# Performance work log

Measured on AMD Instinct MI355X. Metric: run time of the kernel, lower is better.

The kernel has to match this reference:

```python
import jax, jax.numpy as jnp
import numpy as np

VERY_NEGATIVE_NUMBER = -1e29

B, TC, TQ, D = 32, 2048, 256, 256


def setup_inputs() -> dict:
    key = jax.random.key(0)
    k1, k2, k3, k4 = jax.random.split(key, 4)
    context_repr = jax.random.normal(k1, (B, TC, D), dtype=jnp.float32)
    question_repr = jax.random.normal(k2, (B, TQ, D), dtype=jnp.float32)
    # lengths in [1, maxlen] so no row is fully masked
    context_len = jax.random.randint(k3, (B,), 1, TC + 1, dtype=jnp.int32)
    question_len = jax.random.randint(k4, (B,), 1, TQ + 1, dtype=jnp.int32)
    return {
        "context_repr": context_repr,
        "question_repr": question_repr,
        "context_len": context_len,
        "question_len": question_len,
    }


def reference(context_repr, question_repr, context_len, question_len):
    dtype = context_repr.dtype
    Tc = context_repr.shape[1]
    Tq = question_repr.shape[1]
    # similarity: dot product over feature dim -> [B, Tc, Tq]
    sim_mat = jnp.einsum("bcd,bqd->bcq", context_repr, question_repr)
    # sequence masks
    cmask = (jnp.arange(Tc)[None, :] < context_len[:, None]).astype(dtype)  # [B,Tc]
    qmask = (jnp.arange(Tq)[None, :] < question_len[:, None]).astype(dtype)  # [B,Tq]
    mask = cmask[:, :, None] * qmask[:, None, :]  # [B,Tc,Tq]
    sim_mat = sim_mat + (1.0 - mask) * VERY_NEGATIVE_NUMBER
    # context-to-query attention
    c2q_prob = jax.nn.softmax(sim_mat, axis=-1)  # [B,Tc,Tq]
    context2query_attention = jnp.einsum("bcq,bqd->bcd", c2q_prob, question_repr)
    # query-to-context attention: row-wise max then softmax over context positions
    q2c_prob = jax.nn.softmax(jnp.max(sim_mat, axis=-1), axis=-1)  # [B,Tc]
    q2c = jnp.einsum("bc,bcd->bd", q2c_prob, context_repr)  # [B,D]
    query2context_attention = jnp.broadcast_to(
        q2c[:, None, :], context2query_attention.shape
    )
    return (context2query_attention, query2context_attention)
```

## Files before the change

kernel.cpp:

```cpp
#include <hip/hip_runtime.h>
#include <hip/hip_fp16.h>

#define DEVI __device__ __forceinline__

typedef float f32x4 __attribute__((ext_vector_type(4)));
typedef float float4v __attribute__((ext_vector_type(4)));
typedef _Float16 f16x8 __attribute__((ext_vector_type(8)));
typedef unsigned short us8 __attribute__((ext_vector_type(8)));

constexpr int NB = 32, TC = 2048, TQ = 256, DD = 256;
constexpr int CR = 64;
constexpr float VNEG = -1e29f;

DEVI unsigned short f2h(float f) {
  _Float16 h = (_Float16)f;
  return __builtin_bit_cast(unsigned short, h);
}
DEVI float h2f(unsigned short u) {
  return (float)__builtin_bit_cast(_Float16, u);
}

DEVI int swz(int row, int cb) { return cb ^ (((row ^ (cb >> 7)) & 7) << 4); }

DEVI f32x4 mfmah(us8 a, us8 b, f32x4 c) {
  return __builtin_amdgcn_mfma_f32_16x16x32_f16(
      __builtin_bit_cast(f16x8, a), __builtin_bit_cast(f16x8, b), c, 0, 0, 0);
}

__global__ void P0(const float* __restrict__ Qg, unsigned short* __restrict__ Qh,
                   unsigned short* __restrict__ QT)
{
  __shared__ unsigned short t[64][72];
  const int bid = blockIdx.x, tid = threadIdx.x;
  const int b = bid >> 4;
  const int q0 = ((bid >> 2) & 3) * 64, d0 = (bid & 3) * 64;
  {
    const int qr = tid >> 2, dp = (tid & 3) * 16;
    const float* src = Qg + ((size_t)b * TQ + q0 + qr) * DD + d0 + dp;
    unsigned short* dst = Qh + ((size_t)b * TQ + q0 + qr) * DD + d0 + dp;
    us8 o0, o1;
#pragma unroll
    for (int i = 0; i < 4; ++i) {
      float4v v = *(const float4v*)(src + i * 4);
#pragma unroll
      for (int j = 0; j < 4; ++j) {
        const unsigned short h = f2h(v[j]);
        t[qr][dp + i * 4 + j] = h;
        if (i < 2) o0[i * 4 + j] = h; else o1[(i - 2) * 4 + j] = h;
      }
    }
    *(us8*)dst = o0;
    *(us8*)(dst + 8) = o1;
  }
  __syncthreads();
  {
    const int dr = tid >> 2, qp = (tid & 3) * 16;
    us8 a, c;
#pragma unroll
    for (int i = 0; i < 8; ++i) a[i] = t[qp + i][dr];
#pragma unroll
    for (int i = 0; i < 8; ++i) c[i] = t[qp + 8 + i][dr];
    unsigned short* dst = QT + ((size_t)b * DD + d0 + dr) * TQ + q0 + qp;
    *(us8*)dst = a;
    *(us8*)(dst + 8) = c;
  }
}

__global__ __launch_bounds__(512, 6)
void kA(const float* __restrict__ Cg, const unsigned short* __restrict__ Qh,
        const unsigned short* __restrict__ QT,
        const int* __restrict__ clenp, const int* __restrict__ qlenp,
        float* __restrict__ out1, float* __restrict__ pnum,
        float* __restrict__ ptM, float* __restrict__ ptD)
{
  __shared__ __align__(16) char lds[32768];
  __shared__ float redM[512];
  __shared__ float redS[512];
  __shared__ float wred[64];
  __shared__ float wexp[64];
  __shared__ float sinv[64];
  char* const bufC = lds;
  char* const bufP = lds;

  const int bid = blockIdx.x;
  const int b = bid & 31;
  const int tile = bid >> 5;
  const int c0 = tile * CR;
  const int tid = threadIdx.x;
  const int l = tid & 63, wid = tid >> 6;
  const int g = l >> 4, lm = l & 15;
  const int clen = clenp[b], qlen = qlenp[b];

  const float* Cb = Cg + (size_t)(b * TC + c0) * DD;
  const unsigned short* Qhb = Qh + (size_t)b * TQ * DD;
  const unsigned short* QTb = QT + (size_t)b * DD * TQ;

  {
    const int r = tid >> 3;
    const int d0 = (tid & 7) * 32;
    const float* src = Cb + (size_t)r * DD + d0;
#pragma unroll
    for (int i = 0; i < 4; ++i) {
      us8 h;
#pragma unroll
      for (int k = 0; k < 8; k += 4) {
        float4v v = *(const float4v*)(src + i * 8 + k);
#pragma unroll
        for (int j = 0; j < 4; ++j) h[k + j] = f2h(v[j]);
      }
      *(us8*)(bufC + r * 512 + swz(r, (d0 + i * 8) * 2)) = h;
    }
  }
  __syncthreads();

  f32x4 acc[4][2];
#pragma unroll
  for (int mt = 0; mt < 4; ++mt)
#pragma unroll
    for (int nt = 0; nt < 2; ++nt) acc[mt][nt] = (f32x4)0.0f;

  us8 bh[2][2];
#pragma unroll
  for (int nt = 0; nt < 2; ++nt)
    bh[0][nt] = *(const us8*)(Qhb + (size_t)(wid * 32 + nt * 16 + lm) * DD + g * 8);
#pragma unroll
  for (int kk = 0; kk < 8; ++kk) {
    const int cur = kk & 1, nxt = cur ^ 1;
    if (kk < 7) {
#pragma unroll
      for (int nt = 0; nt < 2; ++nt)
        bh[nxt][nt] = *(const us8*)(Qhb + (size_t)(wid * 32 + nt * 16 + lm) * DD +
                                    (kk + 1) * 32 + g * 8);
    }
    us8 ah[4];
#pragma unroll
    for (int mt = 0; mt < 4; ++mt) {
      const int row = mt * 16 + lm;
      ah[mt] = *(const us8*)(bufC + row * 512 + swz(row, kk * 64 + g * 16));
    }
#pragma unroll
    for (int mt = 0; mt < 4; ++mt)
#pragma unroll
      for (int nt = 0; nt < 2; ++nt)
        acc[mt][nt] = mfmah(ah[mt], bh[cur][nt], acc[mt][nt]);
  }

#pragma unroll
  for (int nt = 0; nt < 2; ++nt) {
    const int q = wid * 32 + nt * 16 + lm;
    const bool qm = q >= qlen;
#pragma unroll
    for (int mt = 0; mt < 4; ++mt)
#pragma unroll
      for (int j = 0; j < 4; ++j) {
        const int c = c0 + mt * 16 + g * 4 + j;
        if (qm || c >= clen) acc[mt][nt][j] = VNEG;
      }
  }

#pragma unroll
  for (int mt = 0; mt < 4; ++mt)
#pragma unroll
    for (int j = 0; j < 4; ++j) {
      float m = fmaxf(acc[mt][0][j], acc[mt][1][j]);
      m = fmaxf(m, __shfl_xor(m, 1, 64));
      m = fmaxf(m, __shfl_xor(m, 2, 64));
      m = fmaxf(m, __shfl_xor(m, 4, 64));
      m = fmaxf(m, __shfl_xor(m, 8, 64));
      if (lm == 0) redM[wid * 64 + mt * 16 + g * 4 + j] = m;
    }
  __syncthreads();

  if (tid < 64) {
    float m = redM[tid];
#pragma unroll
    for (int w = 1; w < 8; ++w) m = fmaxf(m, redM[w * 64 + tid]);
    wred[tid] = m;
  }
  __syncthreads();

#pragma unroll
  for (int mt = 0; mt < 4; ++mt)
#pragma unroll
    for (int j = 0; j < 4; ++j) {
      const float m = wred[mt * 16 + g * 4 + j];
      float s = 0.f;
#pragma unroll
      for (int nt = 0; nt < 2; ++nt) {
        const float p = __expf(acc[mt][nt][j] - m);
        acc[mt][nt][j] = p;
        s += p;
      }
      s += __shfl_xor(s, 1, 64);
      s += __shfl_xor(s, 2, 64);
      s += __shfl_xor(s, 4, 64);
      s += __shfl_xor(s, 8, 64);
      if (lm == 0) redS[wid * 64 + mt * 16 + g * 4 + j] = s;
    }
  if (wid == 0) {
    float m = wred[l];
    m = fmaxf(m, __shfl_xor(m, 1, 64));  m = fmaxf(m, __shfl_xor(m, 2, 64));
    m = fmaxf(m, __shfl_xor(m, 4, 64));  m = fmaxf(m, __shfl_xor(m, 8, 64));
    m = fmaxf(m, __shfl_xor(m, 16, 64)); m = fmaxf(m, __shfl_xor(m, 32, 64));
    const float wv = __expf(wred[l] - m);
    wexp[l] = wv;
    float s = wv;
    s += __shfl_xor(s, 1, 64);  s += __shfl_xor(s, 2, 64);
    s += __shfl_xor(s, 4, 64);  s += __shfl_xor(s, 8, 64);
    s += __shfl_xor(s, 16, 64); s += __shfl_xor(s, 32, 64);
    if (l == 0) { ptD[b * 32 + tile] = s; ptM[b * 32 + tile] = m; }
  }
  __syncthreads();

  if (tid < 64) {
    float s = 0.f;
#pragma unroll
    for (int w = 0; w < 8; ++w) s += redS[w * 64 + tid];
    sinv[tid] = 1.0f / s;
  }

  {
    const int half = tid >> 8;
    const int d = tid & 255;
    float qacc = 0.f;
    const int d2 = d * 2;
#pragma unroll 8
    for (int r = half * 32; r < half * 32 + 32; ++r) {
      const float cv = h2f(*(const unsigned short*)(bufC + r * 512 + swz(r, d2)));
      qacc += wexp[r] * cv;
    }
    pnum[(((size_t)b * 32 + tile) * 2 + half) * DD + d] = qacc;
  }
  __syncthreads();

#pragma unroll
  for (int mt = 0; mt < 4; ++mt)
#pragma unroll
    for (int nt = 0; nt < 2; ++nt)
#pragma unroll
      for (int j = 0; j < 4; ++j) {
        const int row = mt * 16 + g * 4 + j;
        const int cb = (wid * 32 + nt * 16 + lm) * 2;
        *(unsigned short*)(bufP + row * 512 + swz(row, cb)) = f2h(acc[mt][nt][j]);
      }
  __syncthreads();

  f32x4 pacc[4][2];
#pragma unroll
  for (int mt = 0; mt < 4; ++mt)
#pragma unroll
    for (int dt = 0; dt < 2; ++dt) pacc[mt][dt] = (f32x4)0.0f;

  us8 qb[2][2];
#pragma unroll
  for (int dt = 0; dt < 2; ++dt)
    qb[0][dt] = *(const us8*)(QTb + (size_t)(wid * 32 + dt * 16 + lm) * TQ + g * 8);
#pragma unroll
  for (int kq = 0; kq < 8; ++kq) {
    const int cur = kq & 1, nxt = cur ^ 1;
    if (kq < 7) {
#pragma unroll
      for (int dt = 0; dt < 2; ++dt)
        qb[nxt][dt] = *(const us8*)(QTb + (size_t)(wid * 32 + dt * 16 + lm) * TQ +
                                    (kq + 1) * 32 + g * 8);
    }
    us8 pa[4];
#pragma unroll
    for (int mt = 0; mt < 4; ++mt) {
      const int row = mt * 16 + lm;
      pa[mt] = *(const us8*)(bufP + row * 512 + swz(row, kq * 64 + g * 16));
    }
#pragma unroll
    for (int mt = 0; mt < 4; ++mt)
#pragma unroll
      for (int dt = 0; dt < 2; ++dt)
        pacc[mt][dt] = mfmah(pa[mt], qb[cur][dt], pacc[mt][dt]);
  }

#pragma unroll
  for (int mt = 0; mt < 4; ++mt)
#pragma unroll
    for (int j = 0; j < 4; ++j) {
      const int row = mt * 16 + g * 4 + j;
      const float inv = sinv[row];
      const size_t rowoff = (size_t)(b * TC + c0 + row) * DD;
#pragma unroll
      for (int dt = 0; dt < 2; ++dt)
        out1[rowoff + wid * 32 + dt * 16 + lm] = pacc[mt][dt][j] * inv;
    }
}

__global__ void kC(const float* __restrict__ pnum, const float* __restrict__ ptM,
                   const float* __restrict__ ptD, float* __restrict__ out2)
{
  const int b = blockIdx.x >> 4, seg = blockIdx.x & 15;
  const int d = threadIdx.x;
  __shared__ float sM[32], sD[32];
  if (d < 32) { sM[d] = ptM[b * 32 + d]; sD[d] = ptD[b * 32 + d]; }
  __syncthreads();
  float m = sM[0];
#pragma unroll
  for (int t = 1; t < 32; ++t) m = fmaxf(m, sM[t]);
  float den = 0.f, acc = 0.f;
#pragma unroll
  for (int t = 0; t < 32; ++t) {
    const float sc = __expf(sM[t] - m);
    den += sc * sD[t];
    const size_t base = (((size_t)b * 32 + t) * 2) * DD + d;
    acc += sc * (pnum[base] + pnum[base + DD]);
  }
  const float s = acc / den;
  float* dst = out2 + ((size_t)b * TC + seg * 128) * DD + d;
#pragma unroll 4
  for (int c = 0; c < 128; ++c) dst[(size_t)c * DD] = s;
}

extern "C" void kernel_launch(void* const* d_in, const int* in_sizes, int n_in,
                              void* d_out, int out_size, void* d_ws, size_t ws_size,
                              hipStream_t stream)
{
  const float* Cg = (const float*)d_in[0];
  const float* Qg = (const float*)d_in[1];
  const int* clen = (const int*)d_in[2];
  const int* qlen = (const int*)d_in[3];
  float* out1 = (float*)d_out;
  float* out2 = out1 + (size_t)NB * TC * DD;

  char* ws = (char*)d_ws;
  float* pnum = (float*)(ws);
  float* ptM  = (float*)(ws + 2097152);
  float* ptD  = (float*)(ws + 2101248);
  unsigned short* Qh = (unsigned short*)(ws + 2105344);
  unsigned short* QT = (unsigned short*)(ws + 2105344 + 4194304);

  P0 <<<dim3(512), dim3(256), 0, stream>>>(Qg, Qh, QT);
  kA <<<dim3(NB * (TC / CR)), dim3(512), 0, stream>>>(Cg, Qh, QT, clen, qlen,
                                                      out1, pnum, ptM, ptD);
  kC <<<dim3(NB * 16), dim3(256), 0, stream>>>(pnum, ptM, ptD, out2);
}
```

Baseline: 83.03 us.

## Raise wave priority around MFMA loops and vectorize q2c broadcast stores

Wraps both MFMA main loops in kA with s_setprio(1)/s_setprio(0) so waves issuing matrix ops get scheduling priority. It also merges the two reduction LDS arrays into one shared buffer to cut LDS footprint. kC switches to float4 loads of the partial numerators and float4 stores of the broadcast output rows, with each thread writing a strided subset of rows. The risk is that kC's launch block size must still be 256 threads for the new row and column indexing to cover everything.

```diff
diff --git a/kernel.cpp b/kernel.cpp
--- a/kernel.cpp
+++ b/kernel.cpp
@@ -74,8 +74,7 @@
         float* __restrict__ ptM, float* __restrict__ ptD)
 {
   __shared__ __align__(16) char lds[32768];
-  __shared__ float redM[512];
-  __shared__ float redS[512];
+  __shared__ float red[512];
   __shared__ float wred[64];
   __shared__ float wexp[64];
   __shared__ float sinv[64];
@@ -91,14 +90,13 @@
   const int g = l >> 4, lm = l & 15;
   const int clen = clenp[b], qlen = qlenp[b];
 
-  const float* Cb = Cg + (size_t)(b * TC + c0) * DD;
   const unsigned short* Qhb = Qh + (size_t)b * TQ * DD;
   const unsigned short* QTb = QT + (size_t)b * DD * TQ;
 
   {
     const int r = tid >> 3;
     const int d0 = (tid & 7) * 32;
-    const float* src = Cb + (size_t)r * DD + d0;
+    const float* src = Cg + (size_t)(b * TC + c0 + r) * DD + d0;
 #pragma unroll
     for (int i = 0; i < 4; ++i) {
       us8 h;
@@ -123,6 +121,7 @@
 #pragma unroll
   for (int nt = 0; nt < 2; ++nt)
     bh[0][nt] = *(const us8*)(Qhb + (size_t)(wid * 32 + nt * 16 + lm) * DD + g * 8);
+  __builtin_amdgcn_s_setprio(1);
 #pragma unroll
   for (int kk = 0; kk < 8; ++kk) {
     const int cur = kk & 1, nxt = cur ^ 1;
@@ -144,6 +143,7 @@
       for (int nt = 0; nt < 2; ++nt)
         acc[mt][nt] = mfmah(ah[mt], bh[cur][nt], acc[mt][nt]);
   }
+  __builtin_amdgcn_s_setprio(0);
 
 #pragma unroll
   for (int nt = 0; nt < 2; ++nt) {
@@ -167,14 +167,14 @@
       m = fmaxf(m, __shfl_xor(m, 2, 64));
       m = fmaxf(m, __shfl_xor(m, 4, 64));
       m = fmaxf(m, __shfl_xor(m, 8, 64));
-      if (lm == 0) redM[wid * 64 + mt * 16 + g * 4 + j] = m;
+      if (lm == 0) red[wid * 64 + mt * 16 + g * 4 + j] = m;
     }
   __syncthreads();
 
   if (tid < 64) {
-    float m = redM[tid];
-#pragma unroll
-    for (int w = 1; w < 8; ++w) m = fmaxf(m, redM[w * 64 + tid]);
+    float m = red[tid];
+#pragma unroll
+    for (int w = 1; w < 8; ++w) m = fmaxf(m, red[w * 64 + tid]);
     wred[tid] = m;
   }
   __syncthreads();
@@ -195,7 +195,7 @@
       s += __shfl_xor(s, 2, 64);
       s += __shfl_xor(s, 4, 64);
       s += __shfl_xor(s, 8, 64);
-      if (lm == 0) redS[wid * 64 + mt * 16 + g * 4 + j] = s;
+      if (lm == 0) red[wid * 64 + mt * 16 + g * 4 + j] = s;
     }
   if (wid == 0) {
     float m = wred[l];
@@ -215,7 +215,7 @@
   if (tid < 64) {
     float s = 0.f;
 #pragma unroll
-    for (int w = 0; w < 8; ++w) s += redS[w * 64 + tid];
+    for (int w = 0; w < 8; ++w) s += red[w * 64 + tid];
     sinv[tid] = 1.0f / s;
   }
 
@@ -251,17 +251,18 @@
 #pragma unroll
     for (int dt = 0; dt < 2; ++dt) pacc[mt][dt] = (f32x4)0.0f;
 
-  us8 qb[2][2];
+  us8 qt[2][2];
 #pragma unroll
   for (int dt = 0; dt < 2; ++dt)
-    qb[0][dt] = *(const us8*)(QTb + (size_t)(wid * 32 + dt * 16 + lm) * TQ + g * 8);
+    qt[0][dt] = *(const us8*)(QTb + (size_t)(wid * 32 + dt * 16 + lm) * TQ + g * 8);
+  __builtin_amdgcn_s_setprio(1);
 #pragma unroll
   for (int kq = 0; kq < 8; ++kq) {
     const int cur = kq & 1, nxt = cur ^ 1;
     if (kq < 7) {
 #pragma unroll
       for (int dt = 0; dt < 2; ++dt)
-        qb[nxt][dt] = *(const us8*)(QTb + (size_t)(wid * 32 + dt * 16 + lm) * TQ +
+        qt[nxt][dt] = *(const us8*)(QTb + (size_t)(wid * 32 + dt * 16 + lm) * TQ +
                                     (kq + 1) * 32 + g * 8);
     }
     us8 pa[4];
@@ -274,8 +275,9 @@
     for (int mt = 0; mt < 4; ++mt)
 #pragma unroll
       for (int dt = 0; dt < 2; ++dt)
-        pacc[mt][dt] = mfmah(pa[mt], qb[cur][dt], pacc[mt][dt]);
-  }
+        pacc[mt][dt] = mfmah(pa[mt], qt[cur][dt], pacc[mt][dt]);
+  }
+  __builtin_amdgcn_s_setprio(0);
 
 #pragma unroll
   for (int mt = 0; mt < 4; ++mt)
@@ -294,25 +296,34 @@
                    const float* __restrict__ ptD, float* __restrict__ out2)
 {
   const int b = blockIdx.x >> 4, seg = blockIdx.x & 15;
-  const int d = threadIdx.x;
+  const int tid = threadIdx.x;
   __shared__ float sM[32], sD[32];
-  if (d < 32) { sM[d] = ptM[b * 32 + d]; sD[d] = ptD[b * 32 + d]; }
+  if (tid < 32) { sM[tid] = ptM[b * 32 + tid]; sD[tid] = ptD[b * 32 + tid]; }
   __syncthreads();
   float m = sM[0];
 #pragma unroll
   for (int t = 1; t < 32; ++t) m = fmaxf(m, sM[t]);
-  float den = 0.f, acc = 0.f;
+  const int d4 = (tid & 63) * 4;
+  float den = 0.f;
+  float4v acc = (float4v)0.0f;
 #pragma unroll
   for (int t = 0; t < 32; ++t) {
     const float sc = __expf(sM[t] - m);
     den += sc * sD[t];
-    const size_t base = (((size_t)b * 32 + t) * 2) * DD + d;
-    acc += sc * (pnum[base] + pnum[base + DD]);
-  }
-  const float s = acc / den;
-  float* dst = out2 + ((size_t)b * TC + seg * 128) * DD + d;
-#pragma unroll 4
-  for (int c = 0; c < 128; ++c) dst[(size_t)c * DD] = s;
+    const size_t base = (((size_t)b * 32 + t) * 2) * DD + d4;
+    const float4v p0 = *(const float4v*)(pnum + base);
+    const float4v p1 = *(const float4v*)(pnum + base + DD);
+#pragma unroll
+    for (int j = 0; j < 4; ++j) acc[j] += sc * (p0[j] + p1[j]);
+  }
+  const float invden = 1.0f / den;
+  float4v sv;
+#pragma unroll
+  for (int j = 0; j < 4; ++j) sv[j] = acc[j] * invden;
+  float* dst = out2 + ((size_t)b * TC + seg * 128) * DD + d4;
+#pragma unroll 8
+  for (int r = (tid >> 6); r < 128; r += 4)
+    *(float4v*)(dst + (size_t)r * DD) = sv;
 }
 
 extern "C" void kernel_launch(void* const* d_in, const int* in_sizes, int n_in,
```

After: 87.03 us. 4.8% more time.
